# Kernel optimization log

Hardware: AMD Instinct MI355X
Metric: run time of the kernel (lower is better)

The kernel has to match this reference:

```python
import jax, jax.numpy as jnp
import numpy as np

ALPHA = 0.2  # LeakyReLU negative slope (pyGAT default)
NEG_INF = -9e15


def setup_inputs() -> dict:
    key = jax.random.key(0)
    ks = jax.random.split(key, 8)
    N, IN, OUT, H, C = 4096, 512, 64, 8, 10
    x = jax.random.normal(ks[0], (N, IN), dtype=jnp.float32)
    adj = jax.random.randint(ks[1], (N, N), 0, 2, dtype=jnp.int32)
    W = jax.random.normal(ks[2], (H, IN, OUT), dtype=jnp.float32) * 0.05
    a1 = jax.random.normal(ks[3], (H, OUT), dtype=jnp.float32) * 0.05
    a2 = jax.random.normal(ks[4], (H, OUT), dtype=jnp.float32) * 0.05
    Wo = jax.random.normal(ks[5], (H * OUT, C), dtype=jnp.float32) * 0.05
    ao1 = jax.random.normal(ks[6], (C,), dtype=jnp.float32) * 0.05
    ao2 = jax.random.normal(ks[7], (C,), dtype=jnp.float32) * 0.05
    return {"x": x, "adj": adj, "W": W, "a1": a1, "a2": a2,
            "Wo": Wo, "ao1": ao1, "ao2": ao2}


def _multi_head_gat(h, mask, W, a1, a2):
    # h: [N, F_in], W: [H, F_in, F_out], a1/a2: [H, F_out], mask: [N, N] bool
    Wh = jnp.einsum('ni,hio->hno', h, W)            # [H, N, F_out]
    f1 = jnp.einsum('hno,ho->hn', Wh, a1)           # [H, N]
    f2 = jnp.einsum('hno,ho->hn', Wh, a2)           # [H, N]
    e = f1[:, :, None] + f2[:, None, :]             # [H, N, N]
    e = jnp.where(e > 0, e, ALPHA * e)              # LeakyReLU(0.2)
    e = jnp.where(mask[None, :, :], e, NEG_INF)     # adjacency mask
    attn = jax.nn.softmax(e, axis=-1)               # [H, N, N]
    return jnp.einsum('hnm,hmo->hno', attn, Wh)     # [H, N, F_out]


def reference(x, adj, W, a1, a2, Wo, ao1, ao2):
    mask = adj > 0
    # hidden heads (concat=True -> ELU on concatenated output)
    heads = _multi_head_gat(x, mask, W, a1, a2)          # [H, N, O]
    H, N, O = heads.shape
    hcat = jnp.transpose(heads, (1, 0, 2)).reshape(N, H * O)
    hcat = jax.nn.elu(hcat)
    # output layer (concat=False -> no ELU)
    out = _multi_head_gat(hcat, mask, Wo[None], ao1[None], ao2[None])[0]  # [N, C]
    return jax.nn.log_softmax(out, axis=-1)
```

## Files before the change

### kernel.cpp

```cpp
#include <hip/hip_runtime.h>
#include <hip/hip_bf16.h>
#include <hip/hip_fp16.h>

typedef __bf16 bf16x8 __attribute__((ext_vector_type(8)));
typedef _Float16 h8_t __attribute__((ext_vector_type(8)));
typedef _Float16 v2h __attribute__((ext_vector_type(2)));
typedef short short8 __attribute__((ext_vector_type(8)));
typedef float f32x4 __attribute__((ext_vector_type(4)));

union BF8 { short8 s; bf16x8 b; };
union H8  { short8 s; h8_t h; unsigned w[4]; };
union HU  { _Float16 f; unsigned short u; };

#define N_NODES 4096
#define F_IN 512
#define F_OUT 64
#define NHEAD 8
#define HID 512
#define NCLS 10
#define GAT_ALPHA 0.2f
#define MSPLIT 4
#define WST 4096
#define NWORD (N_NODES / 64)
#define RB 32
#define CB 64
#define NIT ((N_NODES / MSPLIT) / CB)
#define RB2 16
#define MS2 8
#define MT2 (N_NODES / MS2 / 64)

#define PACK_BLOCKS (N_NODES * NWORD / 4)
#define XCVT_BLOCKS (N_NODES * F_IN / 8 / 256)
#define WCVT_BLOCKS (NHEAD * F_OUT * F_IN / 8 / 256)

#if defined(__has_builtin)
#if __has_builtin(__builtin_amdgcn_fdot2)
#define FDOT2(a, b, c) __builtin_amdgcn_fdot2((a), (b), (c), false)
#endif
#endif
#ifndef FDOT2
#define FDOT2(a, b, c) ((c) + (float)(a)[0] * (float)(b)[0] + (float)(a)[1] * (float)(b)[1])
#endif

__device__ inline unsigned short f2bf(float f) {
  unsigned u = __builtin_bit_cast(unsigned, f);
  unsigned r = (u + 0x7FFFu + ((u >> 16) & 1u)) >> 16;
  return (unsigned short)r;
}
__device__ inline float bf2f(unsigned short h) {
  unsigned u = ((unsigned)h) << 16;
  return __builtin_bit_cast(float, u);
}

__global__ __launch_bounds__(256) void pack_prep_kernel(
    const int* __restrict__ adj, unsigned long long* __restrict__ bits,
    const float* __restrict__ x, unsigned short* __restrict__ xbf,
    const float* __restrict__ W, unsigned short* __restrict__ Wt) {
  const int b = blockIdx.x;
  const int tid = threadIdx.x;
  if (b < PACK_BLOCKS) {
    int wid = b * 4 + (tid >> 6);
    int l = tid & 63;
    unsigned long long m = __ballot(adj[(size_t)wid * 64 + l] != 0);
    if (l == 0) bits[wid] = m;
  } else if (b < PACK_BLOCKS + XCVT_BLOCKS) {
    int idx = (b - PACK_BLOCKS) * 256 + tid;
    const float* src = x + (size_t)idx * 8;
    float4 v0 = *(const float4*)src;
    float4 v1 = *(const float4*)(src + 4);
    short8 sv;
    sv[0]=f2bf(v0.x); sv[1]=f2bf(v0.y); sv[2]=f2bf(v0.z); sv[3]=f2bf(v0.w);
    sv[4]=f2bf(v1.x); sv[5]=f2bf(v1.y); sv[6]=f2bf(v1.z); sv[7]=f2bf(v1.w);
    *(short8*)&xbf[(size_t)idx * 8] = sv;
  } else {
    int t2 = (b - PACK_BLOCKS - XCVT_BLOCKS) * 256 + tid;
    int h   = t2 >> 12;
    int rem = t2 & 4095;
    int o   = rem >> 6;
    int k8  = rem & 63;
    const float* src = W + ((size_t)(h * F_IN) + k8 * 8) * F_OUT + o;
    short8 sv;
    #pragma unroll
    for (int j = 0; j < 8; ++j) sv[j] = (short)f2bf(src[(size_t)j * F_OUT]);
    *(short8*)&Wt[((size_t)(h * F_OUT) + o) * F_IN + k8 * 8] = sv;
  }
}

__global__ __launch_bounds__(256) void gemm1_kernel(
    const unsigned short* __restrict__ xbf, const unsigned short* __restrict__ Wt,
    const float* __restrict__ a1, const float* __restrict__ a2,
    unsigned short* __restrict__ WhbT, float* __restrict__ rho1,
    unsigned short* __restrict__ E2f16, unsigned short* __restrict__ E2sf16) {
  __shared__ __align__(16) short As[4 * 512];
  __shared__ __align__(16) short Bs[4 * 512];
  __shared__ short Ts[64 * 72];
  const int bx = blockIdx.x;
  const int h  = blockIdx.y;
  const int t  = threadIdx.x;
  const int w  = t >> 6, l = t & 63;
  const int lr = l & 15, ls = l >> 4;
  const unsigned short* asrc = xbf + (size_t)(bx * 64 + w * 16 + lr) * F_IN + ls * 8;
  const unsigned short* bsrc = Wt + (size_t)(h * F_OUT + w * 16 + lr) * F_IN + ls * 8;
  f32x4 acc[4] = {};
  __builtin_amdgcn_global_load_lds(
      (const __attribute__((address_space(1))) void*)asrc,
      (__attribute__((address_space(3))) void*)&As[w * 512], 16, 0, 0);
  __builtin_amdgcn_global_load_lds(
      (const __attribute__((address_space(1))) void*)bsrc,
      (__attribute__((address_space(3))) void*)&Bs[w * 512], 16, 0, 0);
  for (int it = 0; it < F_IN / 32; ++it) {
    asm volatile("s_waitcnt vmcnt(0)" ::: "memory");
    __syncthreads();
    BF8 a, b0, b1, b2, b3;
    a.s  = *(short8*)&As[w * 512 + l * 8];
    b0.s = *(short8*)&Bs[0 * 512 + l * 8];
    b1.s = *(short8*)&Bs[1 * 512 + l * 8];
    b2.s = *(short8*)&Bs[2 * 512 + l * 8];
    b3.s = *(short8*)&Bs[3 * 512 + l * 8];
    asm volatile("s_waitcnt lgkmcnt(0)" ::: "memory");
    __syncthreads();
    if (it + 1 < F_IN / 32) {
      __builtin_amdgcn_global_load_lds(
          (const __attribute__((address_space(1))) void*)(asrc + (it + 1) * 32),
          (__attribute__((address_space(3))) void*)&As[w * 512], 16, 0, 0);
      __builtin_amdgcn_global_load_lds(
          (const __attribute__((address_space(1))) void*)(bsrc + (it + 1) * 32),
          (__attribute__((address_space(3))) void*)&Bs[w * 512], 16, 0, 0);
    }
    acc[0] = __builtin_amdgcn_mfma_f32_16x16x32_bf16(a.b, b0.b, acc[0], 0, 0, 0);
    acc[1] = __builtin_amdgcn_mfma_f32_16x16x32_bf16(a.b, b1.b, acc[1], 0, 0, 0);
    acc[2] = __builtin_amdgcn_mfma_f32_16x16x32_bf16(a.b, b2.b, acc[2], 0, 0, 0);
    acc[3] = __builtin_amdgcn_mfma_f32_16x16x32_bf16(a.b, b3.b, acc[3], 0, 0, 0);
  }
  #pragma unroll
  for (int fc = 0; fc < 4; ++fc)
    #pragma unroll
    for (int j = 0; j < 4; ++j) {
      HU hu; hu.f = (_Float16)acc[fc][j];
      Ts[(fc * 16 + lr) * 72 + (w * 16 + ls * 4 + j)] = (short)hu.u;
    }
  __syncthreads();
  {
    int col = t >> 2, seg = t & 3;
    short8 o0 = *(short8*)&Ts[col * 72 + seg * 16];
    short8 o1 = *(short8*)&Ts[col * 72 + seg * 16 + 8];
    unsigned short* dst = WhbT + (size_t)(h * F_OUT + col) * WST + bx * 64 + seg * 16;
    *(short8*)dst = o0;
    *(short8*)(dst + 8) = o1;
  }
  float a1c[4], a2c[4];
  #pragma unroll
  for (int fc = 0; fc < 4; ++fc) {
    a1c[fc] = a1[h * F_OUT + fc * 16 + lr];
    a2c[fc] = a2[h * F_OUT + fc * 16 + lr];
  }
  #pragma unroll
  for (int j = 0; j < 4; ++j) {
    float s1 = 0.f, s2 = 0.f;
    #pragma unroll
    for (int fc = 0; fc < 4; ++fc) { s1 += acc[fc][j] * a1c[fc]; s2 += acc[fc][j] * a2c[fc]; }
    #pragma unroll
    for (int off = 1; off <= 8; off <<= 1) {
      s1 += __shfl_xor(s1, off, 64);
      s2 += __shfl_xor(s2, off, 64);
    }
    if (lr == 0) {
      int row = bx * 64 + w * 16 + ls * 4 + j;
      int idx = h * N_NODES + row;
      rho1[idx] = __expf((GAT_ALPHA - 1.f) * s1);
      HU u1; u1.f = (_Float16)__expf(s2);
      HU u2; u2.f = (_Float16)__expf(GAT_ALPHA * s2);
      E2f16[idx]  = u1.u;
      E2sf16[idx] = u2.u;
    }
  }
}

__global__ __launch_bounds__(512, 4) void att1_kernel(
    const unsigned long long* __restrict__ adjbits,
    const float* __restrict__ rho1,
    const unsigned short* __restrict__ E2f16, const unsigned short* __restrict__ E2sf16,
    const unsigned short* __restrict__ WhbT,
    float* __restrict__ accP, float* __restrict__ SP) {
  __shared__ __align__(16) short Bt[NHEAD][64 * CB];
  const int nb = blockIdx.x * RB;
  const int q  = blockIdx.y;
  const int t  = threadIdx.x;
  const int h  = t >> 6;
  const int l  = t & 63;
  const int r  = l & 15, s = l >> 4;

  const float rho0  = rho1[h * N_NODES + nb + r];
  const float rho1v = rho1[h * N_NODES + nb + 16 + r];
  const v2h rh0 = {(_Float16)rho0, (_Float16)rho0};
  const v2h rh1 = {(_Float16)rho1v, (_Float16)rho1v};
  const v2h ones = {(_Float16)1.0f, (_Float16)1.0f};
  const unsigned short* __restrict__ E2h  = E2f16  + h * N_NODES;
  const unsigned short* __restrict__ E2sh = E2sf16 + h * N_NODES;
  const unsigned long long* __restrict__ ab0 = adjbits + (size_t)(nb + r) * NWORD;
  const unsigned long long* __restrict__ ab1 = adjbits + (size_t)(nb + 16 + r) * NWORD;

  const unsigned short* gsrc0 =
      WhbT + (size_t)(h * F_OUT + (l >> 3)) * WST + (((l & 7) ^ (l >> 3)) * 8);

  const int tb0 = q * (N_NODES / MSPLIT);

  #pragma unroll
  for (int i = 0; i < 8; ++i)
    __builtin_amdgcn_global_load_lds(
        (const __attribute__((address_space(1))) void*)(gsrc0 + tb0 + (size_t)(i * 8) * WST),
        (__attribute__((address_space(3))) void*)&Bt[h][i * 512], 16, 0, 0);

  float S0 = 0.f, S1 = 0.f;
  f32x4 acc[2][4] = {};
  for (int it = 0; it < NIT; ++it) {
    const int tb = tb0 + it * CB;
    const unsigned long long mk0 = ab0[tb >> 6];
    const unsigned long long mk1 = ab1[tb >> 6];
    H8 a0[2], a1f[2];
    #pragma unroll
    for (int kf = 0; kf < 2; ++kf) {
      const int cb = tb + kf * 32 + s * 8;
      uint4 ew = *(const uint4*)(E2h + cb);
      uint4 sw = *(const uint4*)(E2sh + cb);
      const unsigned ewa[4] = {ew.x, ew.y, ew.z, ew.w};
      const unsigned swa[4] = {sw.x, sw.y, sw.z, sw.w};
      const unsigned bm0 = (unsigned)(mk0 >> (kf * 32 + s * 8)) & 0xffu;
      const unsigned bm1 = (unsigned)(mk1 >> (kf * 32 + s * 8)) & 0xffu;
      #pragma unroll
      for (int p = 0; p < 4; ++p) {
        const v2h e2 = __builtin_bit_cast(v2h, ewa[p]);
        const v2h es = __builtin_bit_cast(v2h, swa[p]);
        const unsigned lo0 = ((bm0 >> (2 * p)) & 1u) ? 0x0000FFFFu : 0u;
        const unsigned hi0 = ((bm0 >> (2 * p + 1)) & 1u) ? 0xFFFF0000u : 0u;
        unsigned q0w = __builtin_bit_cast(unsigned, __builtin_elementwise_max(e2, (v2h)(rh0 * es))) & (lo0 | hi0);
        S0 = FDOT2(__builtin_bit_cast(v2h, q0w), ones, S0);
        a0[kf].w[p] = q0w;
        const unsigned lo1 = ((bm1 >> (2 * p)) & 1u) ? 0x0000FFFFu : 0u;
        const unsigned hi1 = ((bm1 >> (2 * p + 1)) & 1u) ? 0xFFFF0000u : 0u;
        unsigned q1w = __builtin_bit_cast(unsigned, __builtin_elementwise_max(e2, (v2h)(rh1 * es))) & (lo1 | hi1);
        S1 = FDOT2(__builtin_bit_cast(v2h, q1w), ones, S1);
        a1f[kf].w[p] = q1w;
      }
    }
    asm volatile("s_waitcnt vmcnt(0)" ::: "memory");
    H8 b[2][4];
    #pragma unroll
    for (int kf = 0; kf < 2; ++kf)
      #pragma unroll
      for (int fc = 0; fc < 4; ++fc)
        b[kf][fc].s = *(short8*)&Bt[h][(fc * 16 + r) * CB + ((kf * 32 + s * 8) ^ ((r & 7) * 8))];
    asm volatile("s_waitcnt lgkmcnt(0)" ::: "memory");
    __builtin_amdgcn_sched_barrier(0);
    if (it + 1 < NIT) {
      #pragma unroll
      for (int i = 0; i < 8; ++i)
        __builtin_amdgcn_global_load_lds(
            (const __attribute__((address_space(1))) void*)(gsrc0 + tb + CB + (size_t)(i * 8) * WST),
            (__attribute__((address_space(3))) void*)&Bt[h][i * 512], 16, 0, 0);
    }
    __builtin_amdgcn_sched_barrier(0);
    #pragma unroll
    for (int kf = 0; kf < 2; ++kf)
      #pragma unroll
      for (int fc = 0; fc < 4; ++fc) {
        acc[0][fc] = __builtin_amdgcn_mfma_f32_16x16x32_f16(a0[kf].h,  b[kf][fc].h, acc[0][fc], 0, 0, 0);
        acc[1][fc] = __builtin_amdgcn_mfma_f32_16x16x32_f16(a1f[kf].h, b[kf][fc].h, acc[1][fc], 0, 0, 0);
      }
  }

  S0 += __shfl_xor(S0, 16, 64); S0 += __shfl_xor(S0, 32, 64);
  S1 += __shfl_xor(S1, 16, 64); S1 += __shfl_xor(S1, 32, 64);
  if (s == 0) {
    SP[((size_t)q * NHEAD + h) * N_NODES + nb + r]      = S0;
    SP[((size_t)q * NHEAD + h) * N_NODES + nb + 16 + r] = S1;
  }
  #pragma unroll
  for (int rg = 0; rg < 2; ++rg)
    #pragma unroll
    for (int fc = 0; fc < 4; ++fc)
      #pragma unroll
      for (int j = 0; j < 4; ++j) {
        int n = nb + rg * 16 + s * 4 + j;
        int col = h * F_OUT + fc * 16 + r;
        accP[((size_t)q * N_NODES + n) * HID + col] = acc[rg][fc][j];
      }
}

__global__ __launch_bounds__(256) void gemm2_kernel(
    const float* __restrict__ accP, const float* __restrict__ SP,
    const float* __restrict__ Wo,
    const float* __restrict__ ao1, const float* __restrict__ ao2,
    unsigned short* __restrict__ Wh2T, float* __restrict__ rho_o,
    float* __restrict__ Eg2, float* __restrict__ Eg2s) {
  int n = blockIdx.x * 4 + (threadIdx.x >> 6);
  int l = threadIdx.x & 63;
  const int h = l >> 3;
  float Ssum = 0.f;
  #pragma unroll
  for (int q = 0; q < MSPLIT; ++q) Ssum += SP[((size_t)q * NHEAD + h) * N_NODES + n];
  float v[8] = {};
  #pragma unroll
  for (int q = 0; q < MSPLIT; ++q) {
    const float* row = accP + ((size_t)q * N_NODES + n) * HID + l * 8;
    float4 va = *(const float4*)row;
    float4 vb = *(const float4*)(row + 4);
    v[0] += va.x; v[1] += va.y; v[2] += va.z; v[3] += va.w;
    v[4] += vb.x; v[5] += vb.y; v[6] += vb.z; v[7] += vb.w;
  }
  float rs = 1.0f / Ssum;
  float acc[NCLS] = {};
  #pragma unroll
  for (int j = 0; j < 8; ++j) {
    float e = v[j] * rs;
    e = e > 0.f ? e : (__expf(e) - 1.0f);
    float hv = bf2f(f2bf(e));
    const float* wrow = Wo + (l * 8 + j) * NCLS;
    #pragma unroll
    for (int c = 0; c < NCLS; ++c) acc[c] += hv * wrow[c];
  }
  #pragma unroll
  for (int c = 0; c < NCLS; ++c)
    #pragma unroll
    for (int off = 32; off > 0; off >>= 1) acc[c] += __shfl_xor(acc[c], off, 64);
  if (l == 0) {
    float s1 = 0.f, s2 = 0.f;
    #pragma unroll
    for (int c = 0; c < NCLS; ++c) {
      s1 += acc[c] * ao1[c];
      s2 += acc[c] * ao2[c];
    }
    #pragma unroll
    for (int c = 0; c < 16; ++c)
      Wh2T[(size_t)c * N_NODES + n] = (c < NCLS) ? f2bf(acc[c]) : (unsigned short)0;
    rho_o[n] = __expf((GAT_ALPHA - 1.f) * s1);
    Eg2[n]   = __expf(s2);
    Eg2s[n]  = __expf(GAT_ALPHA * s2);
  }
}

__global__ __launch_bounds__(512) void att2_kernel(
    const unsigned long long* __restrict__ adjbits,
    const float* __restrict__ rho_o,
    const float* __restrict__ Eg2, const float* __restrict__ Eg2s,
    const unsigned short* __restrict__ Wh2T, float* __restrict__ out) {
  __shared__ float Lacc[MS2][RB2][16];
  __shared__ float LS[MS2][RB2];
  const int nb = blockIdx.x * RB2;
  const int t  = threadIdx.x;
  const int w  = t >> 6;
  const int l  = t & 63;
  const int r  = l & 15, s = l >> 4;
  const int row = nb + r;
  const float ro = rho_o[row];
  const unsigned long long* __restrict__ ab = adjbits + (size_t)row * NWORD;
  const int tb0 = w * (N_NODES / MS2);

  float S = 0.f;
  f32x4 acc = {};
  for (int it = 0; it < MT2; ++it) {
    const int tb = tb0 + it * 64;
    const unsigned long long mk = ab[tb >> 6];
    BF8 a0[2], b0[2];
    #pragma unroll
    for (int kf = 0; kf < 2; ++kf) {
      const int cb = tb + kf * 32 + s * 8;
      b0[kf].s = *(const short8*)(Wh2T + (size_t)r * N_NODES + cb);
      float4 ea = *(const float4*)(Eg2 + cb);
      float4 eb = *(const float4*)(Eg2 + cb + 4);
      float4 sa = *(const float4*)(Eg2s + cb);
      float4 sb = *(const float4*)(Eg2s + cb + 4);
      float ev[8] = {ea.x, ea.y, ea.z, ea.w, eb.x, eb.y, eb.z, eb.w};
      float sv[8] = {sa.x, sa.y, sa.z, sa.w, sb.x, sb.y, sb.z, sb.w};
      const unsigned bm = (unsigned)(mk >> (kf * 32 + s * 8)) & 0xffu;
      #pragma unroll
      for (int j = 0; j < 8; ++j) {
        float qv = fmaxf(ev[j], ro * sv[j]);
        qv = ((bm >> j) & 1u) ? qv : 0.f;
        S += qv;
        a0[kf].b[j] = (__bf16)qv;
      }
    }
    #pragma unroll
    for (int kf = 0; kf < 2; ++kf)
      acc = __builtin_amdgcn_mfma_f32_16x16x32_bf16(a0[kf].b, b0[kf].b, acc, 0, 0, 0);
  }
  S += __shfl_xor(S, 16, 64);
  S += __shfl_xor(S, 32, 64);
  if (s == 0) LS[w][r] = S;
  #pragma unroll
  for (int j = 0; j < 4; ++j) Lacc[w][s * 4 + j][r] = acc[j];
  __syncthreads();
  if (t < 256) {
    const int rr = t >> 4, cc = t & 15;
    float Ssum = 0.f, vsum = 0.f;
    #pragma unroll
    for (int q = 0; q < MS2; ++q) { Ssum += LS[q][rr]; vsum += Lacc[q][rr][cc]; }
    float lo = vsum / Ssum;
    float lom = (cc < NCLS) ? lo : -1e30f;
    float mx = lom;
    #pragma unroll
    for (int off = 1; off <= 8; off <<= 1) mx = fmaxf(mx, __shfl_xor(mx, off, 64));
    float ex = (cc < NCLS) ? __expf(lo - mx) : 0.f;
    float se = ex;
    #pragma unroll
    for (int off = 1; off <= 8; off <<= 1) se += __shfl_xor(se, off, 64);
    float lse = mx + __logf(se);
    if (cc < NCLS) out[(size_t)(nb + rr) * NCLS + cc] = lo - lse;
  }
}

extern "C" void kernel_launch(void* const* d_in, const int* in_sizes, int n_in,
                              void* d_out, int out_size, void* d_ws, size_t ws_size,
                              hipStream_t stream) {
  (void)in_sizes; (void)n_in; (void)out_size; (void)ws_size;
  const float* x   = (const float*)d_in[0];
  const int*   adj = (const int*)d_in[1];
  const float* W   = (const float*)d_in[2];
  const float* a1  = (const float*)d_in[3];
  const float* a2  = (const float*)d_in[4];
  const float* Wo  = (const float*)d_in[5];
  const float* ao1 = (const float*)d_in[6];
  const float* ao2 = (const float*)d_in[7];
  float* out = (float*)d_out;

  char* ws = (char*)d_ws;
  unsigned long long* adjbits = (unsigned long long*)ws; ws += (size_t)N_NODES * NWORD * 8;
  unsigned short* WhbT= (unsigned short*)ws; ws += (size_t)HID * WST * 2;
  float* accP         = (float*)ws;          ws += (size_t)MSPLIT * N_NODES * HID * 4;
  float* SP           = (float*)ws;          ws += (size_t)MSPLIT * NHEAD * N_NODES * 4;
  float* rho1         = (float*)ws;          ws += (size_t)NHEAD * N_NODES * 4;
  unsigned short* E2f16  = (unsigned short*)ws; ws += (size_t)NHEAD * N_NODES * 2;
  unsigned short* E2sf16 = (unsigned short*)ws; ws += (size_t)NHEAD * N_NODES * 2;
  unsigned short* Wh2T= (unsigned short*)ws; ws += (size_t)16 * N_NODES * 2;
  float* rho_o        = (float*)ws;          ws += (size_t)N_NODES * 4;
  float* Eg2          = (float*)ws;          ws += (size_t)N_NODES * 4;
  float* Eg2s         = (float*)ws;          ws += (size_t)N_NODES * 4;
  unsigned short* xbf = (unsigned short*)ws; ws += (size_t)N_NODES * F_IN * 2;
  unsigned short* Wt  = (unsigned short*)ws; ws += (size_t)NHEAD * F_OUT * F_IN * 2;

  pack_prep_kernel<<<PACK_BLOCKS + XCVT_BLOCKS + WCVT_BLOCKS, 256, 0, stream>>>(
      adj, adjbits, x, xbf, W, Wt);
  gemm1_kernel<<<dim3(64, 8), 256, 0, stream>>>(xbf, Wt, a1, a2, WhbT, rho1, E2f16, E2sf16);
  att1_kernel<<<dim3(N_NODES / RB, MSPLIT), 512, 0, stream>>>(adjbits, rho1, E2f16, E2sf16, WhbT, accP, SP);
  gemm2_kernel<<<N_NODES / 4, 256, 0, stream>>>(accP, SP, Wo, ao1, ao2, Wh2T, rho_o, Eg2, Eg2s);
  att2_kernel<<<N_NODES / RB2, 512, 0, stream>>>(adjbits, rho_o, Eg2, Eg2s, Wh2T, out);
}
```

Measured before the change: 113.0 us.

## Share LDS Wh tiles across two row groups, split M by 8, store partials as fp16

The attention-1 kernel now runs 1024-thread blocks that cover 64 rows. Only the first half of the waves issues the async global-to-LDS loads of each Wh tile, and the other half reuses that tile, which halves tile fetches per row. Block-wide barriers are added around the tile reads and refills to keep the shared buffer consistent. MSPLIT doubles to 8 for more column parallelism, and the partial accumulators are written as fp16 instead of fp32 so the partial traffic does not double. This adds barrier cost, precision loss in the partial sums, and a larger reduction in gemm2.

```diff
diff --git a/kernel.cpp b/kernel.cpp
--- a/kernel.cpp
+++ b/kernel.cpp
@@ -19,10 +19,10 @@
 #define HID 512
 #define NCLS 10
 #define GAT_ALPHA 0.2f
-#define MSPLIT 4
+#define MSPLIT 8
 #define WST 4096
 #define NWORD (N_NODES / 64)
-#define RB 32
+#define RBLK 64
 #define CB 64
 #define NIT ((N_NODES / MSPLIT) / CB)
 #define RB2 16
@@ -176,17 +176,19 @@
   }
 }
 
-__global__ __launch_bounds__(512, 4) void att1_kernel(
+__global__ __launch_bounds__(1024, 2) void att1_kernel(
     const unsigned long long* __restrict__ adjbits,
     const float* __restrict__ rho1,
     const unsigned short* __restrict__ E2f16, const unsigned short* __restrict__ E2sf16,
     const unsigned short* __restrict__ WhbT,
-    float* __restrict__ accP, float* __restrict__ SP) {
+    unsigned short* __restrict__ accPh, float* __restrict__ SP) {
   __shared__ __align__(16) short Bt[NHEAD][64 * CB];
-  const int nb = blockIdx.x * RB;
   const int q  = blockIdx.y;
   const int t  = threadIdx.x;
-  const int h  = t >> 6;
+  const int wl = t >> 6;
+  const int h  = wl & 7;
+  const int half = wl >> 3;
+  const int nb = blockIdx.x * RBLK + half * 32;
   const int l  = t & 63;
   const int r  = l & 15, s = l >> 4;
 
@@ -204,12 +206,15 @@
       WhbT + (size_t)(h * F_OUT + (l >> 3)) * WST + (((l & 7) ^ (l >> 3)) * 8);
 
   const int tb0 = q * (N_NODES / MSPLIT);
-
-  #pragma unroll
-  for (int i = 0; i < 8; ++i)
-    __builtin_amdgcn_global_load_lds(
-        (const __attribute__((address_space(1))) void*)(gsrc0 + tb0 + (size_t)(i * 8) * WST),
-        (__attribute__((address_space(3))) void*)&Bt[h][i * 512], 16, 0, 0);
+  const bool issuer = (half == 0);
+
+  if (issuer) {
+    #pragma unroll
+    for (int i = 0; i < 8; ++i)
+      __builtin_amdgcn_global_load_lds(
+          (const __attribute__((address_space(1))) void*)(gsrc0 + tb0 + (size_t)(i * 8) * WST),
+          (__attribute__((address_space(3))) void*)&Bt[h][i * 512], 16, 0, 0);
+  }
 
   float S0 = 0.f, S1 = 0.f;
   f32x4 acc[2][4] = {};
@@ -244,6 +249,7 @@
       }
     }
     asm volatile("s_waitcnt vmcnt(0)" ::: "memory");
+    __syncthreads();
     H8 b[2][4];
     #pragma unroll
     for (int kf = 0; kf < 2; ++kf)
@@ -252,7 +258,8 @@
         b[kf][fc].s = *(short8*)&Bt[h][(fc * 16 + r) * CB + ((kf * 32 + s * 8) ^ ((r & 7) * 8))];
     asm volatile("s_waitcnt lgkmcnt(0)" ::: "memory");
     __builtin_amdgcn_sched_barrier(0);
-    if (it + 1 < NIT) {
+    __syncthreads();
+    if (issuer && it + 1 < NIT) {
       #pragma unroll
       for (int i = 0; i < 8; ++i)
         __builtin_amdgcn_global_load_lds(
@@ -283,12 +290,13 @@
       for (int j = 0; j < 4; ++j) {
         int n = nb + rg * 16 + s * 4 + j;
         int col = h * F_OUT + fc * 16 + r;
-        accP[((size_t)q * N_NODES + n) * HID + col] = acc[rg][fc][j];
+        HU hu; hu.f = (_Float16)acc[rg][fc][j];
+        accPh[((size_t)q * N_NODES + n) * HID + col] = hu.u;
       }
 }
 
 __global__ __launch_bounds__(256) void gemm2_kernel(
-    const float* __restrict__ accP, const float* __restrict__ SP,
+    const unsigned short* __restrict__ accPh, const float* __restrict__ SP,
     const float* __restrict__ Wo,
     const float* __restrict__ ao1, const float* __restrict__ ao2,
     unsigned short* __restrict__ Wh2T, float* __restrict__ rho_o,
@@ -302,11 +310,9 @@
   float v[8] = {};
   #pragma unroll
   for (int q = 0; q < MSPLIT; ++q) {
-    const float* row = accP + ((size_t)q * N_NODES + n) * HID + l * 8;
-    float4 va = *(const float4*)row;
-    float4 vb = *(const float4*)(row + 4);
-    v[0] += va.x; v[1] += va.y; v[2] += va.z; v[3] += va.w;
-    v[4] += vb.x; v[5] += vb.y; v[6] += vb.z; v[7] += vb.w;
+    H8 u; u.s = *(const short8*)&accPh[((size_t)q * N_NODES + n) * HID + l * 8];
+    #pragma unroll
+    for (int j = 0; j < 8; ++j) v[j] += (float)u.h[j];
   }
   float rs = 1.0f / Ssum;
   float acc[NCLS] = {};
@@ -427,7 +433,7 @@
   char* ws = (char*)d_ws;
   unsigned long long* adjbits = (unsigned long long*)ws; ws += (size_t)N_NODES * NWORD * 8;
   unsigned short* WhbT= (unsigned short*)ws; ws += (size_t)HID * WST * 2;
-  float* accP         = (float*)ws;          ws += (size_t)MSPLIT * N_NODES * HID * 4;
+  unsigned short* accPh = (unsigned short*)ws; ws += (size_t)MSPLIT * N_NODES * HID * 2;
   float* SP           = (float*)ws;          ws += (size_t)MSPLIT * NHEAD * N_NODES * 4;
   float* rho1         = (float*)ws;          ws += (size_t)NHEAD * N_NODES * 4;
   unsigned short* E2f16  = (unsigned short*)ws; ws += (size_t)NHEAD * N_NODES * 2;
@@ -442,7 +448,7 @@
   pack_prep_kernel<<<PACK_BLOCKS + XCVT_BLOCKS + WCVT_BLOCKS, 256, 0, stream>>>(
       adj, adjbits, x, xbf, W, Wt);
   gemm1_kernel<<<dim3(64, 8), 256, 0, stream>>>(xbf, Wt, a1, a2, WhbT, rho1, E2f16, E2sf16);
-  att1_kernel<<<dim3(N_NODES / RB, MSPLIT), 512, 0, stream>>>(adjbits, rho1, E2f16, E2sf16, WhbT, accP, SP);
-  gemm2_kernel<<<N_NODES / 4, 256, 0, stream>>>(accP, SP, Wo, ao1, ao2, Wh2T, rho_o, Eg2, Eg2s);
+  att1_kernel<<<dim3(N_NODES / RBLK, MSPLIT), 1024, 0, stream>>>(adjbits, rho1, E2f16, E2sf16, WhbT, accPh, SP);
+  gemm2_kernel<<<N_NODES / 4, 256, 0, stream>>>(accPh, SP, Wo, ao1, ao2, Wh2T, rho_o, Eg2, Eg2s);
   att2_kernel<<<N_NODES / RB2, 512, 0, stream>>>(adjbits, rho_o, Eg2, Eg2s, Wh2T, out);
 }
```

New measurement: 120.9 us. 7.1% more time.
